# Optimization experiments

Hardware: AMD Instinct MI355X
Metric: run time of the kernel (lower is better)

## Reference

```python
import jax, jax.numpy as jnp
import numpy as np

EPS = 1e-12  # matches torch F.normalize default eps


def _l2norm(x):
    # F.normalize(x, dim=-1): x / max(||x||, eps)
    n = jnp.sqrt(jnp.sum(x * x, axis=-1, keepdims=True))
    return x / jnp.maximum(n, EPS)


def setup_inputs() -> dict:
    key = jax.random.key(0)
    kq, kk, kv = jax.random.split(key, 3)
    B, H, N, D = 8, 16, 1024, 64
    q = jax.random.normal(kq, (B, H, N, D), dtype=jnp.float32)
    k = jax.random.normal(kk, (B, H, N, D), dtype=jnp.float32)
    v = jax.random.normal(kv, (B, H, N, D), dtype=jnp.float32)
    return {"q": q, "k": k, "v": v}


def reference(q, k, v):
    B, H, N, D = q.shape
    qn = _l2norm(q)  # [B,H,N,D]
    kn = _l2norm(k)  # [B,H,N,D]
    # cosine-similarity attention logits: [B,H,N,N]
    attn = jnp.einsum("bhnd,bhmd->bhnm", qn, kn)
    attn = jax.nn.softmax(attn, axis=-1)
    # attn_drop is identity (p=0)
    x = jnp.einsum("bhnm,bhmd->bhnd", attn, v)  # [B,H,N,D]
    # transpose(1,2).reshape(B, -1, H*D)
    x = jnp.transpose(x, (0, 2, 1, 3)).reshape(B, N, H * D)
    return x
```

## Files before the change

### kernel.cpp

```cpp
#include <hip/hip_runtime.h>
#include <stdint.h>

typedef __attribute__((ext_vector_type(8))) short short8;
typedef __attribute__((ext_vector_type(4))) float floatx4;

#define B_   8
#define H_   16
#define N_   1024
#define D_   64
#define NH_  (B_*H_)
#define LOG2E 1.44269504088896340736f

extern "C" {
__device__ float __ocml_native_exp2_f32(float);
__device__ float __ocml_native_rsqrt_f32(float);
}

__device__ __forceinline__ unsigned int pk2(float a, float b) {
    unsigned int ua = __float_as_uint(a) + 0x8000u;
    unsigned int ub = __float_as_uint(b) + 0x8000u;
    return __builtin_amdgcn_perm(ub, ua, 0x07060302);
}

__global__ __launch_bounds__(512, 4) void attn_fused(
    const float* __restrict__ q, const float* __restrict__ k,
    const float* __restrict__ v, float* __restrict__ out)
{
    __shared__ __align__(16) unsigned short ks[2][64 * 64];
    __shared__ __align__(16) unsigned short vt[2][64 * 64];

    const int bid = blockIdx.x;
    const int xcd = bid & 7, rest = bid >> 3;
    const int qt = rest & 3;
    const int head = (rest >> 2) * 8 + xcd;
    const int tid = threadIdx.x, w = tid >> 6, lane = tid & 63;
    const int lam = lane & 15, quad = lane >> 4;
    const int sw = lam & 7;
    const int q0 = qt * 256 + w * 32;

    const float* qh = q + ((size_t)head * N_ + q0) * D_;
    const float* kh = k + (size_t)head * N_ * D_;
    const float* vh = v + (size_t)head * N_ * D_;

    short8 aq[2][2];
    #pragma unroll
    for (int t = 0; t < 2; t++) {
        const float* qr = qh + (t * 16 + lam) * D_ + quad * 8;
        float4 f0 = *(const float4*)(qr);
        float4 f1 = *(const float4*)(qr + 4);
        float4 f2 = *(const float4*)(qr + 32);
        float4 f3 = *(const float4*)(qr + 36);
        float ss = f0.x*f0.x + f0.y*f0.y + f0.z*f0.z + f0.w*f0.w
                 + f1.x*f1.x + f1.y*f1.y + f1.z*f1.z + f1.w*f1.w
                 + f2.x*f2.x + f2.y*f2.y + f2.z*f2.z + f2.w*f2.w
                 + f3.x*f3.x + f3.y*f3.y + f3.z*f3.z + f3.w*f3.w;
        ss += __shfl_xor(ss, 16);
        ss += __shfl_xor(ss, 32);
        float sc = LOG2E * __ocml_native_rsqrt_f32(ss);
        union { unsigned int u[4]; short8 s8; } p0, p1;
        p0.u[0] = pk2(f0.x*sc, f0.y*sc); p0.u[1] = pk2(f0.z*sc, f0.w*sc);
        p0.u[2] = pk2(f1.x*sc, f1.y*sc); p0.u[3] = pk2(f1.z*sc, f1.w*sc);
        p1.u[0] = pk2(f2.x*sc, f2.y*sc); p1.u[1] = pk2(f2.z*sc, f2.w*sc);
        p1.u[2] = pk2(f3.x*sc, f3.y*sc); p1.u[3] = pk2(f3.z*sc, f3.w*sc);
        aq[t][0] = p0.s8; aq[t][1] = p1.s8;
    }

    floatx4 oacc[2][4];
    #pragma unroll
    for (int t = 0; t < 2; t++)
        #pragma unroll
        for (int dt = 0; dt < 4; dt++) oacc[t][dt] = (floatx4){0.f, 0.f, 0.f, 0.f};
    float l[2] = {0.f, 0.f};

    const int srow = w * 8 + (lane >> 3);
    const int cbk  = lane & 7;
    const int ksw  = srow & 7;
    const int Lb   = ((w >> 2) << 5) + ((w & 3) << 2);
    const int vwin = (w ^ (lane & 7)) << 3;

    float4 kx[2];
    float  vr[8];

    auto gload = [&](int ck) {
        const float* kp = kh + ((size_t)(ck * 64 + srow)) * D_ + cbk * 8;
        kx[0] = *(const float4*)(kp);
        kx[1] = *(const float4*)(kp + 4);
        #pragma unroll
        for (int j = 0; j < 8; j++) {
            int L = Lb + ((j >> 2) << 4) + (j & 3);
            vr[j] = vh[((size_t)(ck * 64 + L)) * D_ + lane];
        }
    };

    auto stage = [&](int buf) {
        float ss = kx[0].x*kx[0].x + kx[0].y*kx[0].y + kx[0].z*kx[0].z + kx[0].w*kx[0].w
                 + kx[1].x*kx[1].x + kx[1].y*kx[1].y + kx[1].z*kx[1].z + kx[1].w*kx[1].w;
        ss += __shfl_xor(ss, 1);
        ss += __shfl_xor(ss, 2);
        ss += __shfl_xor(ss, 4);
        float sc = __ocml_native_rsqrt_f32(ss);
        union { unsigned int u[4]; short8 s8; } pk;
        pk.u[0] = pk2(kx[0].x*sc, kx[0].y*sc); pk.u[1] = pk2(kx[0].z*sc, kx[0].w*sc);
        pk.u[2] = pk2(kx[1].x*sc, kx[1].y*sc); pk.u[3] = pk2(kx[1].z*sc, kx[1].w*sc);
        *(short8*)&ks[buf][srow * 64 + ((cbk ^ ksw) << 3)] = pk.s8;
        union { unsigned int u[4]; short8 s8; } pv;
        pv.u[0] = pk2(vr[0], vr[1]); pv.u[1] = pk2(vr[2], vr[3]);
        pv.u[2] = pk2(vr[4], vr[5]); pv.u[3] = pk2(vr[6], vr[7]);
        *(short8*)&vt[buf][lane * 64 + vwin] = pv.s8;
    };

    auto compute = [&](int buf) {
        const unsigned short* ksb = &ks[buf][0];
        const unsigned short* vsb = &vt[buf][0];
        #pragma unroll
        for (int g = 0; g < 2; g++) {
            floatx4 s[2][2];
            #pragma unroll
            for (int s2 = 0; s2 < 2; s2++) {
                int st = g * 2 + s2;
                short8 bk0 = *(const short8*)(ksb + (st * 16 + lam) * 64 + (((0 + quad) ^ sw) << 3));
                short8 bk1 = *(const short8*)(ksb + (st * 16 + lam) * 64 + (((4 + quad) ^ sw) << 3));
                #pragma unroll
                for (int t = 0; t < 2; t++) {
                    floatx4 acc = (floatx4){0.f, 0.f, 0.f, 0.f};
                    acc = __builtin_amdgcn_mfma_f32_16x16x32_bf16(bk0, aq[t][0], acc, 0, 0, 0);
                    acc = __builtin_amdgcn_mfma_f32_16x16x32_bf16(bk1, aq[t][1], acc, 0, 0, 0);
                    s[t][s2] = acc;
                }
            }
            short8 pa[2];
            #pragma unroll
            for (int t = 0; t < 2; t++) {
                float e00 = __ocml_native_exp2_f32(s[t][0][0]);
                float e01 = __ocml_native_exp2_f32(s[t][0][1]);
                float e02 = __ocml_native_exp2_f32(s[t][0][2]);
                float e03 = __ocml_native_exp2_f32(s[t][0][3]);
                float e10 = __ocml_native_exp2_f32(s[t][1][0]);
                float e11 = __ocml_native_exp2_f32(s[t][1][1]);
                float e12 = __ocml_native_exp2_f32(s[t][1][2]);
                float e13 = __ocml_native_exp2_f32(s[t][1][3]);
                l[t] += ((e00 + e01) + (e02 + e03)) + ((e10 + e11) + (e12 + e13));
                union { unsigned int u[4]; short8 s8; } pk;
                pk.u[0] = pk2(e00, e01); pk.u[1] = pk2(e02, e03);
                pk.u[2] = pk2(e10, e11); pk.u[3] = pk2(e12, e13);
                pa[t] = pk.s8;
            }
            #pragma unroll
            for (int dt = 0; dt < 4; dt++) {
                short8 bv = *(const short8*)(vsb + (dt * 16 + lam) * 64 + (((g * 4 + quad) ^ sw) << 3));
                #pragma unroll
                for (int t = 0; t < 2; t++)
                    oacc[t][dt] = __builtin_amdgcn_mfma_f32_16x16x32_bf16(pa[t], bv, oacc[t][dt], 0, 0, 0);
            }
        }
    };

    gload(0);
    stage(0);
    __syncthreads();
    for (int c = 0; c < 16; ++c) {
        int buf = c & 1;
        if (c < 15) gload(c + 1);
        compute(buf);
        if (c < 15) stage(buf ^ 1);
        __syncthreads();
    }

    const int b = head >> 4, hh = head & 15;
    #pragma unroll
    for (int t = 0; t < 2; t++) {
        float lr = l[t];
        lr += __shfl_xor(lr, 16);
        lr += __shfl_xor(lr, 32);
        float rl = 1.0f / lr;
        float rq[4];
        #pragma unroll
        for (int r = 0; r < 4; r++) rq[r] = __shfl(rl, quad * 4 + r);
        float* ob = out + ((size_t)b * N_ + q0 + t * 16) * (H_ * D_) + hh * 64;
        #pragma unroll
        for (int dt = 0; dt < 4; dt++)
            #pragma unroll
            for (int r = 0; r < 4; r++)
                ob[(quad * 4 + r) * (H_ * D_) + dt * 16 + lam] = oacc[t][dt][r] * rq[r];
    }
}

extern "C" void kernel_launch(void* const* d_in, const int* in_sizes, int n_in,
                              void* d_out, int out_size, void* d_ws, size_t ws_size,
                              hipStream_t stream) {
    const float* q = (const float*)d_in[0];
    const float* k = (const float*)d_in[1];
    const float* v = (const float*)d_in[2];
    float* out = (float*)d_out;
    (void)d_ws; (void)ws_size;
    hipLaunchKernelGGL(attn_fused, dim3(NH_ * 4), dim3(512), 0, stream, q, k, v, out);
}
```

Before: 159.5 us.

## Precompute normalized bf16 K/V LDS images and DMA them directly into LDS

New measurement: 165.7 us. +3.9%, slower.

```diff
diff --git a/kernel.cpp b/kernel.cpp
--- a/kernel.cpp
+++ b/kernel.cpp
@@ -10,6 +10,8 @@
 #define D_   64
 #define NH_  (B_*H_)
 #define LOG2E 1.44269504088896340736f
+#define IMG_SHORTS 4096
+#define NCHUNK 16
 
 extern "C" {
 __device__ float __ocml_native_exp2_f32(float);
@@ -22,9 +24,56 @@
     return __builtin_amdgcn_perm(ub, ua, 0x07060302);
 }
 
-__global__ __launch_bounds__(512, 4) void attn_fused(
-    const float* __restrict__ q, const float* __restrict__ k,
-    const float* __restrict__ v, float* __restrict__ out)
+
+__global__ __launch_bounds__(512) void prep_kv(
+    const float* __restrict__ k, const float* __restrict__ v,
+    unsigned short* __restrict__ kimg, unsigned short* __restrict__ vimg)
+{
+    const int bid = blockIdx.x;
+    const int head = bid >> 4, ck = bid & 15;
+    const int tid = threadIdx.x, w = tid >> 6, lane = tid & 63;
+
+    const float* kh = k + (size_t)head * N_ * D_;
+    const float* vh = v + (size_t)head * N_ * D_;
+    unsigned short* kd = kimg + ((size_t)(head * 16 + ck)) * IMG_SHORTS;
+    unsigned short* vd = vimg + ((size_t)(head * 16 + ck)) * IMG_SHORTS;
+
+    const int srow = w * 8 + (lane >> 3);
+    const int cbk  = lane & 7;
+    const int ksw  = srow & 7;
+    const float* kp = kh + ((size_t)(ck * 64 + srow)) * D_ + cbk * 8;
+    float4 kx0 = *(const float4*)(kp);
+    float4 kx1 = *(const float4*)(kp + 4);
+    float ss = kx0.x*kx0.x + kx0.y*kx0.y + kx0.z*kx0.z + kx0.w*kx0.w
+             + kx1.x*kx1.x + kx1.y*kx1.y + kx1.z*kx1.z + kx1.w*kx1.w;
+    ss += __shfl_xor(ss, 1);
+    ss += __shfl_xor(ss, 2);
+    ss += __shfl_xor(ss, 4);
+    float sc = __ocml_native_rsqrt_f32(ss);
+    union { unsigned int u[4]; short8 s8; } pk;
+    pk.u[0] = pk2(kx0.x*sc, kx0.y*sc); pk.u[1] = pk2(kx0.z*sc, kx0.w*sc);
+    pk.u[2] = pk2(kx1.x*sc, kx1.y*sc); pk.u[3] = pk2(kx1.z*sc, kx1.w*sc);
+    *(short8*)&kd[srow * 64 + ((cbk ^ ksw) << 3)] = pk.s8;
+
+    const int Lb   = ((w >> 2) << 5) + ((w & 3) << 2);
+    const int vwin = (w ^ (lane & 7)) << 3;
+    float vr[8];
+    #pragma unroll
+    for (int j = 0; j < 8; j++) {
+        int L = Lb + ((j >> 2) << 4) + (j & 3);
+        vr[j] = vh[((size_t)(ck * 64 + L)) * D_ + lane];
+    }
+    union { unsigned int u[4]; short8 s8; } pv;
+    pv.u[0] = pk2(vr[0], vr[1]); pv.u[1] = pk2(vr[2], vr[3]);
+    pv.u[2] = pk2(vr[4], vr[5]); pv.u[3] = pk2(vr[6], vr[7]);
+    *(short8*)&vd[lane * 64 + vwin] = pv.s8;
+}
+
+__global__ __launch_bounds__(512, 4) void attn_fused2(
+    const float* __restrict__ q,
+    const unsigned short* __restrict__ kimg,
+    const unsigned short* __restrict__ vimg,
+    float* __restrict__ out)
 {
     __shared__ __align__(16) unsigned short ks[2][64 * 64];
     __shared__ __align__(16) unsigned short vt[2][64 * 64];
@@ -39,8 +88,8 @@
     const int q0 = qt * 256 + w * 32;
 
     const float* qh = q + ((size_t)head * N_ + q0) * D_;
-    const float* kh = k + (size_t)head * N_ * D_;
-    const float* vh = v + (size_t)head * N_ * D_;
+    const unsigned short* kih = kimg + (size_t)head * 16 * IMG_SHORTS;
+    const unsigned short* vih = vimg + (size_t)head * 16 * IMG_SHORTS;
 
     short8 aq[2][2];
     #pragma unroll
@@ -72,6 +121,145 @@
         for (int dt = 0; dt < 4; dt++) oacc[t][dt] = (floatx4){0.f, 0.f, 0.f, 0.f};
     float l[2] = {0.f, 0.f};
 
+    unsigned short* kw0 = &ks[0][w * 512];
+    unsigned short* kw1 = &ks[1][w * 512];
+    unsigned short* vw0 = &vt[0][w * 512];
+    unsigned short* vw1 = &vt[1][w * 512];
+    auto stage_dma = [&](int buf, int ck) {
+        const unsigned short* kg = kih + ck * IMG_SHORTS + tid * 8;
+        const unsigned short* vg = vih + ck * IMG_SHORTS + tid * 8;
+        __builtin_amdgcn_global_load_lds(
+            reinterpret_cast<const unsigned int*>(kg),
+            reinterpret_cast<unsigned int*>(buf ? kw1 : kw0), 16, 0, 0);
+        __builtin_amdgcn_global_load_lds(
+            reinterpret_cast<const unsigned int*>(vg),
+            reinterpret_cast<unsigned int*>(buf ? vw1 : vw0), 16, 0, 0);
+    };
+
+    auto compute = [&](int buf) {
+        const unsigned short* ksb = &ks[buf][0];
+        const unsigned short* vsb = &vt[buf][0];
+        #pragma unroll
+        for (int g = 0; g < 2; g++) {
+            floatx4 s[2][2];
+            #pragma unroll
+            for (int s2 = 0; s2 < 2; s2++) {
+                int st = g * 2 + s2;
+                short8 bk0 = *(const short8*)(ksb + (st * 16 + lam) * 64 + (((0 + quad) ^ sw) << 3));
+                short8 bk1 = *(const short8*)(ksb + (st * 16 + lam) * 64 + (((4 + quad) ^ sw) << 3));
+                #pragma unroll
+                for (int t = 0; t < 2; t++) {
+                    floatx4 acc = (floatx4){0.f, 0.f, 0.f, 0.f};
+                    acc = __builtin_amdgcn_mfma_f32_16x16x32_bf16(bk0, aq[t][0], acc, 0, 0, 0);
+                    acc = __builtin_amdgcn_mfma_f32_16x16x32_bf16(bk1, aq[t][1], acc, 0, 0, 0);
+                    s[t][s2] = acc;
+                }
+            }
+            short8 pa[2];
+            #pragma unroll
+            for (int t = 0; t < 2; t++) {
+                float e00 = __ocml_native_exp2_f32(s[t][0][0]);
+                float e01 = __ocml_native_exp2_f32(s[t][0][1]);
+                float e02 = __ocml_native_exp2_f32(s[t][0][2]);
+                float e03 = __ocml_native_exp2_f32(s[t][0][3]);
+                float e10 = __ocml_native_exp2_f32(s[t][1][0]);
+                float e11 = __ocml_native_exp2_f32(s[t][1][1]);
+                float e12 = __ocml_native_exp2_f32(s[t][1][2]);
+                float e13 = __ocml_native_exp2_f32(s[t][1][3]);
+                l[t] += ((e00 + e01) + (e02 + e03)) + ((e10 + e11) + (e12 + e13));
+                union { unsigned int u[4]; short8 s8; } pk;
+                pk.u[0] = pk2(e00, e01); pk.u[1] = pk2(e02, e03);
+                pk.u[2] = pk2(e10, e11); pk.u[3] = pk2(e12, e13);
+                pa[t] = pk.s8;
+            }
+            #pragma unroll
+            for (int dt = 0; dt < 4; dt++) {
+                short8 bv = *(const short8*)(vsb + (dt * 16 + lam) * 64 + (((g * 4 + quad) ^ sw) << 3));
+                #pragma unroll
+                for (int t = 0; t < 2; t++)
+                    oacc[t][dt] = __builtin_amdgcn_mfma_f32_16x16x32_bf16(pa[t], bv, oacc[t][dt], 0, 0, 0);
+            }
+        }
+    };
+
+    stage_dma(0, 0);
+    __syncthreads();
+    for (int c = 0; c < 16; ++c) {
+        int buf = c & 1;
+        if (c < 15) stage_dma(buf ^ 1, c + 1);
+        compute(buf);
+        __syncthreads();
+    }
+
+    const int b = head >> 4, hh = head & 15;
+    #pragma unroll
+    for (int t = 0; t < 2; t++) {
+        float lr = l[t];
+        lr += __shfl_xor(lr, 16);
+        lr += __shfl_xor(lr, 32);
+        float rl = 1.0f / lr;
+        float rq[4];
+        #pragma unroll
+        for (int r = 0; r < 4; r++) rq[r] = __shfl(rl, quad * 4 + r);
+        float* ob = out + ((size_t)b * N_ + q0 + t * 16) * (H_ * D_) + hh * 64;
+        #pragma unroll
+        for (int dt = 0; dt < 4; dt++)
+            #pragma unroll
+            for (int r = 0; r < 4; r++)
+                ob[(quad * 4 + r) * (H_ * D_) + dt * 16 + lam] = oacc[t][dt][r] * rq[r];
+    }
+}
+
+__global__ __launch_bounds__(512, 4) void attn_fused(
+    const float* __restrict__ q, const float* __restrict__ k,
+    const float* __restrict__ v, float* __restrict__ out)
+{
+    __shared__ __align__(16) unsigned short ks[2][64 * 64];
+    __shared__ __align__(16) unsigned short vt[2][64 * 64];
+
+    const int bid = blockIdx.x;
+    const int xcd = bid & 7, rest = bid >> 3;
+    const int qt = rest & 3;
+    const int head = (rest >> 2) * 8 + xcd;
+    const int tid = threadIdx.x, w = tid >> 6, lane = tid & 63;
+    const int lam = lane & 15, quad = lane >> 4;
+    const int sw = lam & 7;
+    const int q0 = qt * 256 + w * 32;
+
+    const float* qh = q + ((size_t)head * N_ + q0) * D_;
+    const float* kh = k + (size_t)head * N_ * D_;
+    const float* vh = v + (size_t)head * N_ * D_;
+
+    short8 aq[2][2];
+    #pragma unroll
+    for (int t = 0; t < 2; t++) {
+        const float* qr = qh + (t * 16 + lam) * D_ + quad * 8;
+        float4 f0 = *(const float4*)(qr);
+        float4 f1 = *(const float4*)(qr + 4);
+        float4 f2 = *(const float4*)(qr + 32);
+        float4 f3 = *(const float4*)(qr + 36);
+        float ss = f0.x*f0.x + f0.y*f0.y + f0.z*f0.z + f0.w*f0.w
+                 + f1.x*f1.x + f1.y*f1.y + f1.z*f1.z + f1.w*f1.w
+                 + f2.x*f2.x + f2.y*f2.y + f2.z*f2.z + f2.w*f2.w
+                 + f3.x*f3.x + f3.y*f3.y + f3.z*f3.z + f3.w*f3.w;
+        ss += __shfl_xor(ss, 16);
+        ss += __shfl_xor(ss, 32);
+        float sc = LOG2E * __ocml_native_rsqrt_f32(ss);
+        union { unsigned int u[4]; short8 s8; } p0, p1;
+        p0.u[0] = pk2(f0.x*sc, f0.y*sc); p0.u[1] = pk2(f0.z*sc, f0.w*sc);
+        p0.u[2] = pk2(f1.x*sc, f1.y*sc); p0.u[3] = pk2(f1.z*sc, f1.w*sc);
+        p1.u[0] = pk2(f2.x*sc, f2.y*sc); p1.u[1] = pk2(f2.z*sc, f2.w*sc);
+        p1.u[2] = pk2(f3.x*sc, f3.y*sc); p1.u[3] = pk2(f3.z*sc, f3.w*sc);
+        aq[t][0] = p0.s8; aq[t][1] = p1.s8;
+    }
+
+    floatx4 oacc[2][4];
+    #pragma unroll
+    for (int t = 0; t < 2; t++)
+        #pragma unroll
+        for (int dt = 0; dt < 4; dt++) oacc[t][dt] = (floatx4){0.f, 0.f, 0.f, 0.f};
+    float l[2] = {0.f, 0.f};
+
     const int srow = w * 8 + (lane >> 3);
     const int cbk  = lane & 7;
     const int ksw  = srow & 7;
@@ -192,6 +380,13 @@
     const float* k = (const float*)d_in[1];
     const float* v = (const float*)d_in[2];
     float* out = (float*)d_out;
-    (void)d_ws; (void)ws_size;
-    hipLaunchKernelGGL(attn_fused, dim3(NH_ * 4), dim3(512), 0, stream, q, k, v, out);
-}
+    const size_t need = (size_t)NH_ * NCHUNK * IMG_SHORTS * 2 * sizeof(unsigned short);
+    if (d_ws != nullptr && ws_size >= need) {
+        unsigned short* kimg = (unsigned short*)d_ws;
+        unsigned short* vimg = kimg + (size_t)NH_ * NCHUNK * IMG_SHORTS;
+        hipLaunchKernelGGL(prep_kv, dim3(NH_ * NCHUNK), dim3(512), 0, stream, k, v, kimg, vimg);
+        hipLaunchKernelGGL(attn_fused2, dim3(NH_ * 4), dim3(512), 0, stream, q, kimg, vimg, out);
+    } else {
+        hipLaunchKernelGGL(attn_fused, dim3(NH_ * 4), dim3(512), 0, stream, q, k, v, out);
+    }
+}
```
